# Kernel optimization log

Measured on AMD Instinct MI355X. Metric: run time of the kernel, lower is better.

Reference implementation:

```python
import jax, jax.numpy as jnp
import numpy as np

HIDDEN = 1024
HEADS = 16
HEAD_SIZE = HIDDEN // HEADS


def setup_inputs() -> dict:
    key = jax.random.key(0)
    k0, k1, k2, k3 = jax.random.split(key, 4)
    scale = 1.0 / np.sqrt(HIDDEN)
    return {
        "input_data": jax.random.normal(k0, (4, 4096, HIDDEN), dtype=jnp.float32),
        "W0": jax.random.normal(k1, (HIDDEN, HIDDEN), dtype=jnp.float32) * scale,
        "W1": jax.random.normal(k2, (HIDDEN, HIDDEN), dtype=jnp.float32) * scale,
        "W2": jax.random.normal(k3, (HIDDEN, HIDDEN), dtype=jnp.float32) * scale,
    }


def reference(input_data, W0, W1, W2):
    b, s, _ = input_data.shape
    k, h = HEADS, HEAD_SIZE
    # torch.nn.Linear(bias=False): y = x @ W.T
    out = input_data @ W0.T          # [b, s, hidden]
    out1 = input_data @ W1.T
    out2 = input_data @ W2.T
    # reshape to heads; cummax over the sequence axis (axis=1 here, which
    # matches cummax(dim=2) on the permuted (b,k,s,h) layout in torch)
    out_h = out.reshape(b, s, k, h)
    out1_h = out1.reshape(b, s, k, h)
    cm = jax.lax.associative_scan(jnp.maximum, (out_h + out1_h) / jnp.sqrt(jnp.float32(h)), axis=1)
    cm = cm.reshape(b, s, k * h)
    out = (cm + out2) * cm + out1
    return out
```

## Files before the change

### kernel.cpp

```cpp
#include <hip/hip_runtime.h>
#include <cstdint>
#include <cstddef>

#define HIDDEN 1024
#define BATCH 4
#define SEQ 4096
#define M_ROWS (BATCH * SEQ)
#define K_DIM 1024
#define SUBCHUNK 32
#define NSUB (SEQ / SUBCHUNK)

typedef __bf16 bf16_t;
typedef __bf16 v8bf __attribute__((ext_vector_type(8)));
typedef float v4f __attribute__((ext_vector_type(4)));

__device__ __forceinline__ unsigned short f32_to_bf16(float f) {
  unsigned int u = __float_as_uint(f);
  u += 0x7fffu + ((u >> 16) & 1u);
  return (unsigned short)(u >> 16);
}
__device__ __forceinline__ float bf16_to_f32(unsigned short u) {
  return __uint_as_float((unsigned int)u << 16);
}

__global__ void convert_kernel(const float* __restrict__ X,
                               const float* __restrict__ W0,
                               const float* __restrict__ W1,
                               const float* __restrict__ W2,
                               unsigned short* __restrict__ Xb,
                               unsigned short* __restrict__ Wb) {
  int bx = blockIdx.x;
  if (bx < 16384) {
    int i = bx * 256 + threadIdx.x;
    float4 f = ((const float4*)X)[i];
    ushort4 u;
    u.x = f32_to_bf16(f.x); u.y = f32_to_bf16(f.y);
    u.z = f32_to_bf16(f.z); u.w = f32_to_bf16(f.w);
    ((ushort4*)Xb)[i] = u;
  } else {
    int i = (bx - 16384) * 256 + threadIdx.x;
    int mat = i >> 18;
    int off = i & 0x3FFFF;
    float4 f;
    if (mat == 0) {
      float4 a = ((const float4*)W0)[off];
      float4 b = ((const float4*)W1)[off];
      f.x = (a.x + b.x) * 0.125f; f.y = (a.y + b.y) * 0.125f;
      f.z = (a.z + b.z) * 0.125f; f.w = (a.w + b.w) * 0.125f;
    } else {
      const float* src = (mat == 1) ? W1 : W2;
      f = ((const float4*)src)[off];
    }
    ushort4 u;
    u.x = f32_to_bf16(f.x); u.y = f32_to_bf16(f.y);
    u.z = f32_to_bf16(f.z); u.w = f32_to_bf16(f.w);
    ((ushort4*)Wb)[i] = u;
  }
}


__global__ __launch_bounds__(512, 2) void gemm_s_kernel(
    const bf16_t* __restrict__ A, const bf16_t* __restrict__ B,
    unsigned short* __restrict__ Lp, float* __restrict__ cmax) {
  extern __shared__ __align__(16) char smem[];

  const int tid = threadIdx.x;
  const int wave = tid >> 6;
  const int lane = tid & 63;
  const int quad = lane >> 4;
  const int r16 = lane & 15;
  const int wr = wave >> 2;
  const int wc = wave & 3;

  const int orig = (int)blockIdx.x;
  const int swz = (orig & 7) * 32 + (orig >> 3);
  const int bx = swz & 3;
  const int mt = swz >> 2;
  const int mtile0 = mt * 256;
  const int nbase = bx * 256;

  const int sr = lane >> 2;
  const int sc = lane & 3;
  const size_t laneOff = (size_t)sr * K_DIM + (size_t)((sc ^ (sr & 3)) << 3);
  const bf16_t* Ag = A + (size_t)(mtile0 + wave * 32) * K_DIM + laneOff;
  const bf16_t* Bg = B + (size_t)(nbase + wave * 32) * K_DIM + laneOff;

  const int aRowB = (wr * 128 + r16) * 64;
  const int bRowB = (wc * 64 + r16) * 64;
  const int kch = (quad ^ (r16 & 3)) << 4;

  v4f acc[8][4];
#pragma unroll
  for (int i = 0; i < 8; ++i)
#pragma unroll
    for (int j = 0; j < 4; ++j) acc[i][j] = (v4f)(0.0f);

  v8bf afr[4];
  v8bf bfr[4];

#define STG_A(sb, st, jj) __builtin_amdgcn_global_load_lds( \
    (__attribute__((address_space(1))) void*)(Ag + (size_t)(st) * 32 + (size_t)(jj) * (16 * K_DIM)), \
    (__attribute__((address_space(3))) void*)(smem + (sb) * 16384 + wave * 2048 + (jj) * 1024), 16, 0, 0)
#define STG_B(sb, st, jj) __builtin_amdgcn_global_load_lds( \
    (__attribute__((address_space(1))) void*)(Bg + (size_t)(st) * 32 + (size_t)(jj) * (16 * K_DIM)), \
    (__attribute__((address_space(3))) void*)(smem + 65536 + (sb) * 16384 + wave * 2048 + (jj) * 1024), 16, 0, 0)
#define LDA(bf, i) (*(const v8bf*)(smem + (bf) * 16384 + aRowB + (i) * 1024 + kch))
#define LDB(bf, j) (*(const v8bf*)(smem + 65536 + (bf) * 16384 + bRowB + (j) * 1024 + kch))
#define BAR() __builtin_amdgcn_s_barrier()
#define WAITV(n) asm volatile("s_waitcnt vmcnt(" #n ")" ::: "memory")

#define BODY(st, bf, DOSTG, WVW) { \
    if (DOSTG) { STG_A((((st) + 3) & 3), (st) + 3, 0); STG_B((((st) + 3) & 3), (st) + 3, 0); } \
    _Pragma("unroll") for (int j = 0; j < 4; ++j) bfr[j] = LDB(bf, j); \
    _Pragma("unroll") for (int i = 0; i < 4; ++i) afr[i] = LDA(bf, i); \
    __builtin_amdgcn_s_setprio(1); \
    _Pragma("unroll") for (int i = 0; i < 4; ++i) \
      _Pragma("unroll") for (int j = 0; j < 4; ++j) \
        acc[i][j] = __builtin_amdgcn_mfma_f32_16x16x32_bf16(afr[i], bfr[j], acc[i][j], 0, 0, 0); \
    __builtin_amdgcn_s_setprio(0); \
    if (DOSTG) { STG_A((((st) + 3) & 3), (st) + 3, 1); STG_B((((st) + 3) & 3), (st) + 3, 1); } \
    _Pragma("unroll") for (int i = 0; i < 4; ++i) afr[i] = LDA(bf, 4 + i); \
    __builtin_amdgcn_s_setprio(1); \
    _Pragma("unroll") for (int i = 0; i < 4; ++i) \
      _Pragma("unroll") for (int j = 0; j < 4; ++j) \
        acc[4 + i][j] = __builtin_amdgcn_mfma_f32_16x16x32_bf16(afr[i], bfr[j], acc[4 + i][j], 0, 0, 0); \
    __builtin_amdgcn_s_setprio(0); \
    WVW; BAR(); }

#pragma unroll
  for (int s = 0; s < 3; ++s) {
    STG_A(s, s, 0); STG_B(s, s, 0);
    STG_A(s, s, 1); STG_B(s, s, 1);
  }
  WAITV(8);
  BAR();

#pragma unroll 1
  for (int g = 0; g < 7; ++g) {
    const int s0 = g * 4;
    BODY(s0 + 0, 0, 1, WAITV(8));
    BODY(s0 + 1, 1, 1, WAITV(8));
    BODY(s0 + 2, 2, 1, WAITV(8));
    BODY(s0 + 3, 3, 1, WAITV(8));
  }
  BODY(28, 0, 1, WAITV(8));
  BODY(29, 1, 0, WAITV(4));
  BODY(30, 2, 0, WAITV(0));
  BODY(31, 3, 0, );

#undef BODY
#undef STG_A
#undef STG_B
#undef LDA
#undef LDB
#undef BAR
#undef WAITV

  const int ncol0 = bx * 256;
  const int bidx = mtile0 >> 12;
  const int sub0 = (mtile0 & 4095) >> 5;
#pragma unroll
  for (int s = 0; s < 4; ++s) {
#pragma unroll
    for (int j = 0; j < 4; ++j) {
      float c0[4], c1[4];
      c0[0] = acc[s * 2][j][0];
      c1[0] = acc[s * 2 + 1][j][0];
#pragma unroll
      for (int r = 1; r < 4; ++r) {
        c0[r] = fmaxf(c0[r - 1], acc[s * 2][j][r]);
        c1[r] = fmaxf(c1[r - 1], acc[s * 2 + 1][j][r]);
      }
      float t0 = c0[3], t1 = c1[3], u;
      u = __shfl_up(t0, 16); if (quad >= 1) t0 = fmaxf(t0, u);
      u = __shfl_up(t0, 32); if (quad >= 2) t0 = fmaxf(t0, u);
      u = __shfl_up(t1, 16); if (quad >= 1) t1 = fmaxf(t1, u);
      u = __shfl_up(t1, 32); if (quad >= 2) t1 = fmaxf(t1, u);
      float e0 = __shfl_up(t0, 16); if (quad == 0) e0 = -INFINITY;
      float e1 = __shfl_up(t1, 16); if (quad == 0) e1 = -INFINITY;
      float T0 = __shfl(t0, 48 + r16);
      float T1 = __shfl(t1, 48 + r16);
      int col = ncol0 + wc * 64 + j * 16 + r16;
      int rowb = mtile0 + wr * 128 + s * 32 + quad * 4;
#pragma unroll
      for (int r = 0; r < 4; ++r) {
        float L0 = fmaxf(c0[r], e0);
        float L1 = fmaxf(fmaxf(c1[r], e1), T0);
        Lp[(size_t)(rowb + r) * HIDDEN + col] = f32_to_bf16(L0);
        Lp[(size_t)(rowb + 16 + r) * HIDDEN + col] = f32_to_bf16(L1);
      }
      if (quad == 0) {
        int sub = sub0 + wr * 4 + s;
        cmax[((size_t)bidx * NSUB + sub) * HIDDEN + col] = fmaxf(T0, T1);
      }
    }
  }
}

__global__ void prefix_kernel(const float* __restrict__ cmax,
                              float* __restrict__ pmax) {
  int col = blockIdx.x * 256 + threadIdx.x;
  int b = blockIdx.y;
  const float* cp = cmax + (size_t)b * NSUB * HIDDEN + col;
  float* pp = pmax + (size_t)b * NSUB * HIDDEN + col;
  float run = -INFINITY;
#pragma unroll 1
  for (int s0 = 0; s0 < NSUB; s0 += 16) {
    float v[16];
#pragma unroll
    for (int i = 0; i < 16; ++i) v[i] = cp[(size_t)(s0 + i) * HIDDEN];
#pragma unroll
    for (int i = 0; i < 16; ++i) {
      pp[(size_t)(s0 + i) * HIDDEN] = run;
      run = fmaxf(run, v[i]);
    }
  }
}

__global__ __launch_bounds__(512, 2) void gemm_f_kernel(
    const bf16_t* __restrict__ A, const bf16_t* __restrict__ B,
    const unsigned short* __restrict__ Lp, const float* __restrict__ pmax,
    float* __restrict__ out) {
  extern __shared__ __align__(16) char smem[];

  const int tid = threadIdx.x;
  const int wave = tid >> 6;
  const int lane = tid & 63;
  const int quad = lane >> 4;
  const int r16 = lane & 15;
  const int wr = wave >> 2;
  const int wc = wave & 3;

  const int orig = (int)blockIdx.x;
  const int swz = (orig & 7) * 64 + (orig >> 3);
  const int mt = swz >> 3;
  const int nt = swz & 7;
  const int mtile0 = mt * 256;
  const int ncol0 = nt * 128;

  const int sr = lane >> 2;
  const int sc = lane & 3;
  const size_t laneOff = (size_t)sr * K_DIM + (size_t)((sc ^ (sr & 3)) << 3);
  const bf16_t* Ag = A + (size_t)(mtile0 + wave * 32) * K_DIM + laneOff;
  const bf16_t* Bg1 = B + (size_t)(1024 + ncol0 + wave * 16) * K_DIM + laneOff;
  const bf16_t* Bg2 = B + (size_t)(2048 + ncol0 + wave * 16) * K_DIM + laneOff;

  const int aRowB = (wr * 128 + r16) * 64;
  const int bRowB = (wc * 32 + r16) * 64;
  const int kch = (quad ^ (r16 & 3)) << 4;

  v4f acc1[8][2], acc2[8][2];
#pragma unroll
  for (int i = 0; i < 8; ++i)
#pragma unroll
    for (int j = 0; j < 2; ++j) { acc1[i][j] = (v4f)(0.0f); acc2[i][j] = (v4f)(0.0f); }

  v8bf afr[4];
  v8bf b1fr[2], b2fr[2];

#define STG2_A(sb, st, jj) __builtin_amdgcn_global_load_lds( \
    (__attribute__((address_space(1))) void*)(Ag + (size_t)(st) * 32 + (size_t)(jj) * (16 * K_DIM)), \
    (__attribute__((address_space(3))) void*)(smem + (sb) * 16384 + wave * 2048 + (jj) * 1024), 16, 0, 0)
#define STG2_B1(sb, st) __builtin_amdgcn_global_load_lds( \
    (__attribute__((address_space(1))) void*)(Bg1 + (size_t)(st) * 32), \
    (__attribute__((address_space(3))) void*)(smem + 65536 + (sb) * 16384 + wave * 1024), 16, 0, 0)
#define STG2_B2(sb, st) __builtin_amdgcn_global_load_lds( \
    (__attribute__((address_space(1))) void*)(Bg2 + (size_t)(st) * 32), \
    (__attribute__((address_space(3))) void*)(smem + 65536 + (sb) * 16384 + 8192 + wave * 1024), 16, 0, 0)
#define LDA2(bf, i) (*(const v8bf*)(smem + (bf) * 16384 + aRowB + (i) * 1024 + kch))
#define LDB1(bf, j) (*(const v8bf*)(smem + 65536 + (bf) * 16384 + bRowB + (j) * 1024 + kch))
#define LDB2(bf, j) (*(const v8bf*)(smem + 65536 + (bf) * 16384 + 8192 + bRowB + (j) * 1024 + kch))
#define BAR() __builtin_amdgcn_s_barrier()
#define WAITV(n) asm volatile("s_waitcnt vmcnt(" #n ")" ::: "memory")

#define BODY2(st, bf, DOSTG, WVW) { \
    if (DOSTG) { STG2_A((((st) + 3) & 3), (st) + 3, 0); STG2_B1((((st) + 3) & 3), (st) + 3); } \
    _Pragma("unroll") for (int j = 0; j < 2; ++j) { b1fr[j] = LDB1(bf, j); b2fr[j] = LDB2(bf, j); } \
    _Pragma("unroll") for (int i = 0; i < 4; ++i) afr[i] = LDA2(bf, i); \
    __builtin_amdgcn_s_setprio(1); \
    _Pragma("unroll") for (int i = 0; i < 4; ++i) \
      _Pragma("unroll") for (int j = 0; j < 2; ++j) { \
        acc1[i][j] = __builtin_amdgcn_mfma_f32_16x16x32_bf16(afr[i], b1fr[j], acc1[i][j], 0, 0, 0); \
        acc2[i][j] = __builtin_amdgcn_mfma_f32_16x16x32_bf16(afr[i], b2fr[j], acc2[i][j], 0, 0, 0); } \
    __builtin_amdgcn_s_setprio(0); \
    if (DOSTG) { STG2_A((((st) + 3) & 3), (st) + 3, 1); STG2_B2((((st) + 3) & 3), (st) + 3); } \
    _Pragma("unroll") for (int i = 0; i < 4; ++i) afr[i] = LDA2(bf, 4 + i); \
    __builtin_amdgcn_s_setprio(1); \
    _Pragma("unroll") for (int i = 0; i < 4; ++i) \
      _Pragma("unroll") for (int j = 0; j < 2; ++j) { \
        acc1[4 + i][j] = __builtin_amdgcn_mfma_f32_16x16x32_bf16(afr[i], b1fr[j], acc1[4 + i][j], 0, 0, 0); \
        acc2[4 + i][j] = __builtin_amdgcn_mfma_f32_16x16x32_bf16(afr[i], b2fr[j], acc2[4 + i][j], 0, 0, 0); } \
    __builtin_amdgcn_s_setprio(0); \
    WVW; BAR(); }

#pragma unroll
  for (int s = 0; s < 3; ++s) {
    STG2_A(s, s, 0); STG2_B1(s, s);
    STG2_A(s, s, 1); STG2_B2(s, s);
  }
  WAITV(8);
  BAR();

#pragma unroll 1
  for (int g = 0; g < 7; ++g) {
    const int s0 = g * 4;
    BODY2(s0 + 0, 0, 1, WAITV(8));
    BODY2(s0 + 1, 1, 1, WAITV(8));
    BODY2(s0 + 2, 2, 1, WAITV(8));
    BODY2(s0 + 3, 3, 1, WAITV(8));
  }
  BODY2(28, 0, 1, WAITV(8));
  BODY2(29, 1, 0, WAITV(4));
  BODY2(30, 2, 0, WAITV(0));
  BODY2(31, 3, 0, );

#undef BODY2
#undef STG2_A
#undef STG2_B1
#undef STG2_B2
#undef LDA2
#undef LDB1
#undef LDB2
#undef BAR
#undef WAITV

  const int bidx = mtile0 >> 12;
  const int sub0 = (mtile0 & 4095) >> 5;
#pragma unroll
  for (int i = 0; i < 8; ++i) {
    const int subr = sub0 + wr * 4 + (i >> 1);
#pragma unroll
    for (int j = 0; j < 2; ++j) {
      const int col = ncol0 + wc * 32 + j * 16 + r16;
      const float pm = pmax[((size_t)bidx * NSUB + subr) * HIDDEN + col];
      const int row0 = mtile0 + wr * 128 + i * 16 + quad * 4;
#pragma unroll
      for (int r = 0; r < 4; ++r) {
        size_t idx = (size_t)(row0 + r) * HIDDEN + col;
        float m = fmaxf(pm, bf16_to_f32(Lp[idx]));
        out[idx] = (m + acc2[i][j][r]) * m + acc1[i][j][r];
      }
    }
  }
}

extern "C" void kernel_launch(void* const* d_in, const int* in_sizes, int n_in,
                              void* d_out, int out_size, void* d_ws, size_t ws_size,
                              hipStream_t stream) {
  const float* X = (const float*)d_in[0];
  const float* W0 = (const float*)d_in[1];
  const float* W1 = (const float*)d_in[2];
  const float* W2 = (const float*)d_in[3];
  float* out = (float*)d_out;

  char* ws = (char*)d_ws;
  unsigned short* Xb = (unsigned short*)ws;
  unsigned short* Wb = (unsigned short*)(ws + 33554432);
  unsigned short* Lp = (unsigned short*)(ws + 33554432 + 6291456);
  float* cmax = (float*)(ws + 4 * 33554432 + 6291456);
  float* pmax = (float*)(ws + 4 * 33554432 + 6291456 + 2097152);

  convert_kernel<<<19456, 256, 0, stream>>>(X, W0, W1, W2, Xb, Wb);

  gemm_s_kernel<<<256, 512, 131072, stream>>>((const bf16_t*)Xb, (const bf16_t*)Wb,
                                              Lp, cmax);

  dim3 pgrid(4, BATCH);
  prefix_kernel<<<pgrid, 256, 0, stream>>>(cmax, pmax);

  gemm_f_kernel<<<512, 512, 131072, stream>>>((const bf16_t*)Xb, (const bf16_t*)Wb,
                                              Lp, pmax, out);
}
```

Before: 137.9 us.

## Load GEMM B fragments directly from global memory and double K-step to 64

Both GEMM kernels stop staging the weight (B) tiles through LDS and instead load each wave's B fragments straight from global memory into registers. The K tile per stage grows from 32 to 64, which halves the number of barrier-separated iterations and doubles A's LDS footprint per buffer; A also gets a new 8-way XOR swizzle. This is meant to cut LDS traffic and barrier count, at the cost of uncoalesced-ish direct global loads for B whose latency is only hidden by the vmcnt waits and L2 reuse across waves.

```diff
diff --git a/kernel.cpp b/kernel.cpp
--- a/kernel.cpp
+++ b/kernel.cpp
@@ -79,15 +79,16 @@
   const int mtile0 = mt * 256;
   const int nbase = bx * 256;
 
-  const int sr = lane >> 2;
-  const int sc = lane & 3;
-  const size_t laneOff = (size_t)sr * K_DIM + (size_t)((sc ^ (sr & 3)) << 3);
-  const bf16_t* Ag = A + (size_t)(mtile0 + wave * 32) * K_DIM + laneOff;
-  const bf16_t* Bg = B + (size_t)(nbase + wave * 32) * K_DIM + laneOff;
-
-  const int aRowB = (wr * 128 + r16) * 64;
-  const int bRowB = (wc * 64 + r16) * 64;
-  const int kch = (quad ^ (r16 & 3)) << 4;
+  const int l3 = lane >> 3;
+  const int lc = lane & 7;
+  const size_t laneOff = (size_t)l3 * K_DIM + (size_t)((lc ^ l3) << 3);
+  const bf16_t* Ag = A + (size_t)(mtile0 + wave * 8) * K_DIM + laneOff;
+
+  const bf16_t* Bg = B + (size_t)(nbase + wc * 64 + r16) * K_DIM + quad * 8;
+
+  const int aRow = (wr * 128 + r16) * 128;
+  const int cxor = (r16 & 7) * 16;
+  const int qx = quad * 16;
 
   v4f acc[8][4];
 #pragma unroll
@@ -96,63 +97,56 @@
     for (int j = 0; j < 4; ++j) acc[i][j] = (v4f)(0.0f);
 
   v8bf afr[4];
-  v8bf bfr[4];
-
-#define STG_A(sb, st, jj) __builtin_amdgcn_global_load_lds( \
-    (__attribute__((address_space(1))) void*)(Ag + (size_t)(st) * 32 + (size_t)(jj) * (16 * K_DIM)), \
-    (__attribute__((address_space(3))) void*)(smem + (sb) * 16384 + wave * 2048 + (jj) * 1024), 16, 0, 0)
-#define STG_B(sb, st, jj) __builtin_amdgcn_global_load_lds( \
-    (__attribute__((address_space(1))) void*)(Bg + (size_t)(st) * 32 + (size_t)(jj) * (16 * K_DIM)), \
-    (__attribute__((address_space(3))) void*)(smem + 65536 + (sb) * 16384 + wave * 2048 + (jj) * 1024), 16, 0, 0)
-#define LDA(bf, i) (*(const v8bf*)(smem + (bf) * 16384 + aRowB + (i) * 1024 + kch))
-#define LDB(bf, j) (*(const v8bf*)(smem + 65536 + (bf) * 16384 + bRowB + (j) * 1024 + kch))
+  v8bf bfr[4][2];
+
+#define STG_A(sb, kt) { _Pragma("unroll") for (int q = 0; q < 4; ++q) \
+    __builtin_amdgcn_global_load_lds( \
+      (__attribute__((address_space(1))) void*)(Ag + (size_t)q * (64 * K_DIM) + (size_t)(kt) * 64), \
+      (__attribute__((address_space(3))) void*)(smem + (sb) * 32768 + q * 8192 + wave * 1024), 16, 0, 0); }
+#define LDA(bf, i, kk) (*(const v8bf*)(smem + (bf) * 32768 + aRow + (i) * 2048 + (((kk) * 64 + qx) ^ cxor)))
+#define LDB_G(j, kk, kt) (*(const v8bf*)(Bg + (size_t)(j) * (16 * K_DIM) + (size_t)(kt) * 64 + (kk) * 32))
 #define BAR() __builtin_amdgcn_s_barrier()
 #define WAITV(n) asm volatile("s_waitcnt vmcnt(" #n ")" ::: "memory")
 
-#define BODY(st, bf, DOSTG, WVW) { \
-    if (DOSTG) { STG_A((((st) + 3) & 3), (st) + 3, 0); STG_B((((st) + 3) & 3), (st) + 3, 0); } \
-    _Pragma("unroll") for (int j = 0; j < 4; ++j) bfr[j] = LDB(bf, j); \
-    _Pragma("unroll") for (int i = 0; i < 4; ++i) afr[i] = LDA(bf, i); \
-    __builtin_amdgcn_s_setprio(1); \
-    _Pragma("unroll") for (int i = 0; i < 4; ++i) \
-      _Pragma("unroll") for (int j = 0; j < 4; ++j) \
-        acc[i][j] = __builtin_amdgcn_mfma_f32_16x16x32_bf16(afr[i], bfr[j], acc[i][j], 0, 0, 0); \
-    __builtin_amdgcn_s_setprio(0); \
-    if (DOSTG) { STG_A((((st) + 3) & 3), (st) + 3, 1); STG_B((((st) + 3) & 3), (st) + 3, 1); } \
-    _Pragma("unroll") for (int i = 0; i < 4; ++i) afr[i] = LDA(bf, 4 + i); \
-    __builtin_amdgcn_s_setprio(1); \
-    _Pragma("unroll") for (int i = 0; i < 4; ++i) \
-      _Pragma("unroll") for (int j = 0; j < 4; ++j) \
-        acc[4 + i][j] = __builtin_amdgcn_mfma_f32_16x16x32_bf16(afr[i], bfr[j], acc[4 + i][j], 0, 0, 0); \
-    __builtin_amdgcn_s_setprio(0); \
+#define BODY(kt, bf, DOSTG, WVW) { \
+    _Pragma("unroll") for (int j = 0; j < 4; ++j) { \
+      bfr[j][0] = LDB_G(j, 0, kt); bfr[j][1] = LDB_G(j, 1, kt); } \
+    if (DOSTG) STG_A((((kt) + 3) & 3), (kt) + 3); \
+    _Pragma("unroll") for (int kk = 0; kk < 2; ++kk) { \
+      _Pragma("unroll") for (int ih = 0; ih < 2; ++ih) { \
+        _Pragma("unroll") for (int i = 0; i < 4; ++i) afr[i] = LDA(bf, ih * 4 + i, kk); \
+        __builtin_amdgcn_s_setprio(1); \
+        _Pragma("unroll") for (int i = 0; i < 4; ++i) \
+          _Pragma("unroll") for (int j = 0; j < 4; ++j) \
+            acc[ih * 4 + i][j] = __builtin_amdgcn_mfma_f32_16x16x32_bf16(afr[i], bfr[j][kk], acc[ih * 4 + i][j], 0, 0, 0); \
+        __builtin_amdgcn_s_setprio(0); } } \
     WVW; BAR(); }
 
-#pragma unroll
-  for (int s = 0; s < 3; ++s) {
-    STG_A(s, s, 0); STG_B(s, s, 0);
-    STG_A(s, s, 1); STG_B(s, s, 1);
-  }
+  STG_A(0, 0); STG_A(1, 1); STG_A(2, 2);
   WAITV(8);
   BAR();
 
+  BODY(0, 0, 1, WAITV(16));
+  BODY(1, 1, 1, WAITV(24));
+  BODY(2, 2, 1, WAITV(24));
+  BODY(3, 3, 1, WAITV(24));
 #pragma unroll 1
-  for (int g = 0; g < 7; ++g) {
+  for (int g = 1; g <= 2; ++g) {
     const int s0 = g * 4;
-    BODY(s0 + 0, 0, 1, WAITV(8));
-    BODY(s0 + 1, 1, 1, WAITV(8));
-    BODY(s0 + 2, 2, 1, WAITV(8));
-    BODY(s0 + 3, 3, 1, WAITV(8));
-  }
-  BODY(28, 0, 1, WAITV(8));
-  BODY(29, 1, 0, WAITV(4));
-  BODY(30, 2, 0, WAITV(0));
-  BODY(31, 3, 0, );
+    BODY(s0 + 0, 0, 1, WAITV(24));
+    BODY(s0 + 1, 1, 1, WAITV(24));
+    BODY(s0 + 2, 2, 1, WAITV(24));
+    BODY(s0 + 3, 3, 1, WAITV(24));
+  }
+  BODY(12, 0, 1, WAITV(24));
+  BODY(13, 1, 0, WAITV(20));
+  BODY(14, 2, 0, WAITV(16));
+  BODY(15, 3, 0, );
 
 #undef BODY
 #undef STG_A
-#undef STG_B
 #undef LDA
-#undef LDB
+#undef LDB_G
 #undef BAR
 #undef WAITV
 
@@ -238,16 +232,17 @@
   const int mtile0 = mt * 256;
   const int ncol0 = nt * 128;
 
-  const int sr = lane >> 2;
-  const int sc = lane & 3;
-  const size_t laneOff = (size_t)sr * K_DIM + (size_t)((sc ^ (sr & 3)) << 3);
-  const bf16_t* Ag = A + (size_t)(mtile0 + wave * 32) * K_DIM + laneOff;
-  const bf16_t* Bg1 = B + (size_t)(1024 + ncol0 + wave * 16) * K_DIM + laneOff;
-  const bf16_t* Bg2 = B + (size_t)(2048 + ncol0 + wave * 16) * K_DIM + laneOff;
-
-  const int aRowB = (wr * 128 + r16) * 64;
-  const int bRowB = (wc * 32 + r16) * 64;
-  const int kch = (quad ^ (r16 & 3)) << 4;
+  const int l3 = lane >> 3;
+  const int lc = lane & 7;
+  const size_t laneOff = (size_t)l3 * K_DIM + (size_t)((lc ^ l3) << 3);
+  const bf16_t* Ag = A + (size_t)(mtile0 + wave * 8) * K_DIM + laneOff;
+
+  const bf16_t* Bg1 = B + (size_t)(1024 + ncol0 + wc * 32 + r16) * K_DIM + quad * 8;
+  const bf16_t* Bg2 = B + (size_t)(2048 + ncol0 + wc * 32 + r16) * K_DIM + quad * 8;
+
+  const int aRow = (wr * 128 + r16) * 128;
+  const int cxor = (r16 & 7) * 16;
+  const int qx = quad * 16;
 
   v4f acc1[8][2], acc2[8][2];
 #pragma unroll
@@ -256,71 +251,60 @@
     for (int j = 0; j < 2; ++j) { acc1[i][j] = (v4f)(0.0f); acc2[i][j] = (v4f)(0.0f); }
 
   v8bf afr[4];
-  v8bf b1fr[2], b2fr[2];
-
-#define STG2_A(sb, st, jj) __builtin_amdgcn_global_load_lds( \
-    (__attribute__((address_space(1))) void*)(Ag + (size_t)(st) * 32 + (size_t)(jj) * (16 * K_DIM)), \
-    (__attribute__((address_space(3))) void*)(smem + (sb) * 16384 + wave * 2048 + (jj) * 1024), 16, 0, 0)
-#define STG2_B1(sb, st) __builtin_amdgcn_global_load_lds( \
-    (__attribute__((address_space(1))) void*)(Bg1 + (size_t)(st) * 32), \
-    (__attribute__((address_space(3))) void*)(smem + 65536 + (sb) * 16384 + wave * 1024), 16, 0, 0)
-#define STG2_B2(sb, st) __builtin_amdgcn_global_load_lds( \
-    (__attribute__((address_space(1))) void*)(Bg2 + (size_t)(st) * 32), \
-    (__attribute__((address_space(3))) void*)(smem + 65536 + (sb) * 16384 + 8192 + wave * 1024), 16, 0, 0)
-#define LDA2(bf, i) (*(const v8bf*)(smem + (bf) * 16384 + aRowB + (i) * 1024 + kch))
-#define LDB1(bf, j) (*(const v8bf*)(smem + 65536 + (bf) * 16384 + bRowB + (j) * 1024 + kch))
-#define LDB2(bf, j) (*(const v8bf*)(smem + 65536 + (bf) * 16384 + 8192 + bRowB + (j) * 1024 + kch))
+  v8bf b1fr[2][2], b2fr[2][2];
+
+#define STG2_A(sb, kt) { _Pragma("unroll") for (int q = 0; q < 4; ++q) \
+    __builtin_amdgcn_global_load_lds( \
+      (__attribute__((address_space(1))) void*)(Ag + (size_t)q * (64 * K_DIM) + (size_t)(kt) * 64), \
+      (__attribute__((address_space(3))) void*)(smem + (sb) * 32768 + q * 8192 + wave * 1024), 16, 0, 0); }
+#define LDA2(bf, i, kk) (*(const v8bf*)(smem + (bf) * 32768 + aRow + (i) * 2048 + (((kk) * 64 + qx) ^ cxor)))
+#define LDB1_G(j, kk, kt) (*(const v8bf*)(Bg1 + (size_t)(j) * (16 * K_DIM) + (size_t)(kt) * 64 + (kk) * 32))
+#define LDB2_G(j, kk, kt) (*(const v8bf*)(Bg2 + (size_t)(j) * (16 * K_DIM) + (size_t)(kt) * 64 + (kk) * 32))
 #define BAR() __builtin_amdgcn_s_barrier()
 #define WAITV(n) asm volatile("s_waitcnt vmcnt(" #n ")" ::: "memory")
 
-#define BODY2(st, bf, DOSTG, WVW) { \
-    if (DOSTG) { STG2_A((((st) + 3) & 3), (st) + 3, 0); STG2_B1((((st) + 3) & 3), (st) + 3); } \
-    _Pragma("unroll") for (int j = 0; j < 2; ++j) { b1fr[j] = LDB1(bf, j); b2fr[j] = LDB2(bf, j); } \
-    _Pragma("unroll") for (int i = 0; i < 4; ++i) afr[i] = LDA2(bf, i); \
-    __builtin_amdgcn_s_setprio(1); \
-    _Pragma("unroll") for (int i = 0; i < 4; ++i) \
-      _Pragma("unroll") for (int j = 0; j < 2; ++j) { \
-        acc1[i][j] = __builtin_amdgcn_mfma_f32_16x16x32_bf16(afr[i], b1fr[j], acc1[i][j], 0, 0, 0); \
-        acc2[i][j] = __builtin_amdgcn_mfma_f32_16x16x32_bf16(afr[i], b2fr[j], acc2[i][j], 0, 0, 0); } \
-    __builtin_amdgcn_s_setprio(0); \
-    if (DOSTG) { STG2_A((((st) + 3) & 3), (st) + 3, 1); STG2_B2((((st) + 3) & 3), (st) + 3); } \
-    _Pragma("unroll") for (int i = 0; i < 4; ++i) afr[i] = LDA2(bf, 4 + i); \
-    __builtin_amdgcn_s_setprio(1); \
-    _Pragma("unroll") for (int i = 0; i < 4; ++i) \
-      _Pragma("unroll") for (int j = 0; j < 2; ++j) { \
-        acc1[4 + i][j] = __builtin_amdgcn_mfma_f32_16x16x32_bf16(afr[i], b1fr[j], acc1[4 + i][j], 0, 0, 0); \
-        acc2[4 + i][j] = __builtin_amdgcn_mfma_f32_16x16x32_bf16(afr[i], b2fr[j], acc2[4 + i][j], 0, 0, 0); } \
-    __builtin_amdgcn_s_setprio(0); \
+#define BODY2(kt, bf, DOSTG, WVW) { \
+    _Pragma("unroll") for (int j = 0; j < 2; ++j) { \
+      b1fr[j][0] = LDB1_G(j, 0, kt); b1fr[j][1] = LDB1_G(j, 1, kt); \
+      b2fr[j][0] = LDB2_G(j, 0, kt); b2fr[j][1] = LDB2_G(j, 1, kt); } \
+    if (DOSTG) STG2_A((((kt) + 3) & 3), (kt) + 3); \
+    _Pragma("unroll") for (int kk = 0; kk < 2; ++kk) { \
+      _Pragma("unroll") for (int ih = 0; ih < 2; ++ih) { \
+        _Pragma("unroll") for (int i = 0; i < 4; ++i) afr[i] = LDA2(bf, ih * 4 + i, kk); \
+        __builtin_amdgcn_s_setprio(1); \
+        _Pragma("unroll") for (int i = 0; i < 4; ++i) \
+          _Pragma("unroll") for (int j = 0; j < 2; ++j) { \
+            acc1[ih * 4 + i][j] = __builtin_amdgcn_mfma_f32_16x16x32_bf16(afr[i], b1fr[j][kk], acc1[ih * 4 + i][j], 0, 0, 0); \
+            acc2[ih * 4 + i][j] = __builtin_amdgcn_mfma_f32_16x16x32_bf16(afr[i], b2fr[j][kk], acc2[ih * 4 + i][j], 0, 0, 0); } \
+        __builtin_amdgcn_s_setprio(0); } } \
     WVW; BAR(); }
 
-#pragma unroll
-  for (int s = 0; s < 3; ++s) {
-    STG2_A(s, s, 0); STG2_B1(s, s);
-    STG2_A(s, s, 1); STG2_B2(s, s);
-  }
+  STG2_A(0, 0); STG2_A(1, 1); STG2_A(2, 2);
   WAITV(8);
   BAR();
 
+  BODY2(0, 0, 1, WAITV(16));
+  BODY2(1, 1, 1, WAITV(24));
+  BODY2(2, 2, 1, WAITV(24));
+  BODY2(3, 3, 1, WAITV(24));
 #pragma unroll 1
-  for (int g = 0; g < 7; ++g) {
+  for (int g = 1; g <= 2; ++g) {
     const int s0 = g * 4;
-    BODY2(s0 + 0, 0, 1, WAITV(8));
-    BODY2(s0 + 1, 1, 1, WAITV(8));
-    BODY2(s0 + 2, 2, 1, WAITV(8));
-    BODY2(s0 + 3, 3, 1, WAITV(8));
-  }
-  BODY2(28, 0, 1, WAITV(8));
-  BODY2(29, 1, 0, WAITV(4));
-  BODY2(30, 2, 0, WAITV(0));
-  BODY2(31, 3, 0, );
+    BODY2(s0 + 0, 0, 1, WAITV(24));
+    BODY2(s0 + 1, 1, 1, WAITV(24));
+    BODY2(s0 + 2, 2, 1, WAITV(24));
+    BODY2(s0 + 3, 3, 1, WAITV(24));
+  }
+  BODY2(12, 0, 1, WAITV(24));
+  BODY2(13, 1, 0, WAITV(20));
+  BODY2(14, 2, 0, WAITV(16));
+  BODY2(15, 3, 0, );
 
 #undef BODY2
 #undef STG2_A
-#undef STG2_B1
-#undef STG2_B2
 #undef LDA2
-#undef LDB1
-#undef LDB2
+#undef LDB1_G
+#undef LDB2_G
 #undef BAR
 #undef WAITV
 
```

Result: slower. 186.8 us (+35.5%).
